# Kernel tuning notes

Hardware: AMD Instinct MI355X
Metric: run time of the kernel (lower is better)

Reference implementation:

```python
import jax, jax.numpy as jnp
import numpy as np

B, Q, MAXK, C, D, H, NL = 64, 16, 32, 64, 768, 512, 2
S = Q * (MAXK + 1) + 1  # max padded sequence length (529)


def lstm_layer(x, w_ih, w_hh, b_ih, b_hh):
    # x: [B, S, Din]; torch gate order i, f, g, o
    xg = jnp.einsum('bsd,gd->bsg', x, w_ih) + b_ih + b_hh  # [B,S,4H]
    h0 = jnp.zeros((x.shape[0], w_hh.shape[1]), x.dtype)

    def step(carry, xt):
        h, c = carry
        g = xt + h @ w_hh.T
        i, f, gg, o = jnp.split(g, 4, axis=-1)
        c = jax.nn.sigmoid(f) * c + jax.nn.sigmoid(i) * jnp.tanh(gg)
        h = jax.nn.sigmoid(o) * jnp.tanh(c)
        return (h, c), h

    _, hs = jax.lax.scan(step, (h0, h0), jnp.swapaxes(xg, 0, 1))
    return jnp.swapaxes(hs, 0, 1)  # [B,S,H]


def build_sequence(text_output, questions_outputs, code_embedding, num_snapshots, que_num):
    # Vectorized equivalent of the nested scatter loops.
    valid_q = jnp.arange(Q)[None, :] < que_num[:, None]          # [B,Q]
    qlen = jnp.where(valid_q, num_snapshots + 1, 0)              # per-question block length
    starts = jnp.cumsum(qlen, axis=1) - qlen                     # exclusive cumsum: block start
    L = jnp.sum(qlen, axis=1)                                    # text position; seq_len = L+1

    buf = jnp.zeros((B, S + 1, D), text_output.dtype)            # extra dump slot at index S
    b1 = jnp.arange(B)[:, None]

    # scatter question embeddings at block starts
    q_dest = jnp.where(valid_q, starts, S)
    buf = buf.at[b1, q_dest].set(questions_outputs)

    # scatter code snapshots: dest = start+1+k, src = code_embedding[b, i+k] (as in source)
    k = jnp.arange(MAXK)
    ns = jnp.where(valid_q, num_snapshots, 0)
    valid_s = k[None, None, :] < ns[:, :, None]                  # [B,Q,K]
    dest = jnp.where(valid_s, starts[:, :, None] + 1 + k[None, None, :], S)
    src = jnp.clip(jnp.arange(Q)[:, None] + k[None, :], 0, C - 1)  # [Q,K]
    code_vals = code_embedding[:, src]                           # [B,Q,K,D]
    buf = buf.at[jnp.arange(B)[:, None, None], dest].set(code_vals)

    # current-question text embedding at end of sequence
    buf = buf.at[jnp.arange(B), L].set(text_output)
    return buf[:, :S], L


def setup_inputs() -> dict:
    key = jax.random.key(0)
    ks = jax.random.split(key, 16)
    inp = {
        'text_output': jax.random.normal(ks[0], (B, D), jnp.float32),
        'questions_outputs': jax.random.normal(ks[1], (B, Q, D), jnp.float32),
        'code_embedding': jax.random.normal(ks[2], (B, C, D), jnp.float32),
        'num_snapshots': jax.random.randint(ks[3], (B, Q), 1, MAXK + 1, jnp.int32),
        'que_num': jax.random.randint(ks[4], (B,), 1, Q + 1, jnp.int32),
    }
    s = 0.02
    inp['w_ih_l0'] = jax.random.normal(ks[5], (4 * H, D), jnp.float32) * s
    inp['w_hh_l0'] = jax.random.normal(ks[6], (4 * H, H), jnp.float32) * s
    inp['b_ih_l0'] = jnp.zeros((4 * H,), jnp.float32)
    inp['b_hh_l0'] = jnp.zeros((4 * H,), jnp.float32)
    inp['w_ih_l1'] = jax.random.normal(ks[7], (4 * H, H), jnp.float32) * s
    inp['w_hh_l1'] = jax.random.normal(ks[8], (4 * H, H), jnp.float32) * s
    inp['b_ih_l1'] = jnp.zeros((4 * H,), jnp.float32)
    inp['b_hh_l1'] = jnp.zeros((4 * H,), jnp.float32)
    inp['fc_w'] = jax.random.normal(ks[9], (1, H), jnp.float32) * s
    inp['fc_b'] = jnp.zeros((1,), jnp.float32)
    return inp


def reference(text_output, questions_outputs, code_embedding, num_snapshots, que_num,
              w_ih_l0, w_hh_l0, b_ih_l0, b_hh_l0,
              w_ih_l1, w_hh_l1, b_ih_l1, b_hh_l1, fc_w, fc_b):
    x, L = build_sequence(text_output, questions_outputs, code_embedding, num_snapshots, que_num)
    h = lstm_layer(x, w_ih_l0, w_hh_l0, b_ih_l0, b_hh_l0)
    h = lstm_layer(h, w_ih_l1, w_hh_l1, b_ih_l1, b_hh_l1)
    last = h[jnp.arange(B), L]  # output at seq_len-1 (= text position)
    return last @ fc_w.T + fc_b  # [B, 1]
```

## Files before the change

kernel.cpp:

```cpp
#include <hip/hip_runtime.h>
#include <hip/hip_cooperative_groups.h>

namespace cg = cooperative_groups;

#define B_    64
#define Q_    16
#define MAXK_ 32
#define C_    64
#define D_    768
#define H_    512
#define G4_   2048
#define S_    529
#define NR_   81

typedef float f32x4_t __attribute__((ext_vector_type(4)));
typedef unsigned int u32x2_t __attribute__((ext_vector_type(2)));
typedef unsigned int u32x4_t __attribute__((ext_vector_type(4)));
typedef _Float16 f16x8_t __attribute__((ext_vector_type(8)));

static constexpr size_t OFF_L     = 0;
static constexpr size_t OFF_MAXL  = 256;
static constexpr size_t OFF_MAP   = 512;
static constexpr size_t OFF_BIAS0 = OFF_MAP   + 135424;
static constexpr size_t OFF_BIAS1 = OFF_BIAS0 + 8192;
static constexpr size_t OFF_C0    = OFF_BIAS1 + 8192;
static constexpr size_t OFF_C1    = OFF_C0    + 131072;
static constexpr size_t OFF_HLAST = OFF_C1    + 131072;
static constexpr size_t OFF_H0B   = OFF_HLAST + 131072;
static constexpr size_t OFF_H1B   = OFF_H0B   + 262144;
static constexpr size_t OFF_WTIH0 = OFF_H1B   + 262144;
static constexpr size_t OFF_XPROJ = OFF_WTIH0 + 6291456ULL;
static constexpr size_t OFF_BAR   = OFF_XPROJ + 42467328ULL;
static constexpr size_t OFF_ORD   = OFF_BAR   + 4096;
static constexpr size_t OFF_GMAX  = OFF_ORD   + 256;
static constexpr size_t WS_NEED   = OFF_GMAX  + 256;

__device__ __forceinline__ int group_base(int g) {
  return (g == 0) ? 0 : (g == 1) ? 16 : (g == 2) ? 48 : 32;
}

__device__ __forceinline__ void store_us_cc(ushort* p, unsigned int v) {
  asm volatile("global_store_short %0, %1, off sc0 sc1" :: "v"(p), "v"(v) : "memory");
}
__device__ __forceinline__ void store_f_cc(float* p, float v) {
  asm volatile("global_store_dword %0, %1, off sc0 sc1" :: "v"(p), "v"(v) : "memory");
}
__device__ __forceinline__ void load_a_cc(u32x4_t& v, const ushort* p) {
  asm volatile("global_load_dwordx4 %0, %1, off sc0 sc1" : "=v"(v) : "v"(p) : "memory");
}

__device__ __forceinline__ unsigned int pkrtz(float a, float b) {
  auto r = __builtin_amdgcn_cvt_pkrtz(a, b);
  unsigned int u;
  __builtin_memcpy(&u, &r, 4);
  return u;
}
__device__ __forceinline__ unsigned int f2h(float a) {
  return pkrtz(a, 0.f) & 0xffffu;
}
__device__ __forceinline__ f32x4_t mfma16(u32x4_t a, u32x4_t b, f32x4_t c) {
  f16x8_t av, bv;
  __builtin_memcpy(&av, &a, 16);
  __builtin_memcpy(&bv, &b, 16);
  return __builtin_amdgcn_mfma_f32_16x16x32_f16(av, bv, c, 0, 0, 0);
}

__device__ __forceinline__ float sigm(float x) { return 1.f/(1.f + __expf(-x)); }

__global__ __launch_bounds__(256) void k_prep(
    const int* __restrict__ ns, const int* __restrict__ que,
    const float* __restrict__ b_ih0, const float* __restrict__ b_hh0,
    const float* __restrict__ b_ih1, const float* __restrict__ b_hh1,
    int* __restrict__ Lp, int* __restrict__ maxLp, int* __restrict__ map,
    float* __restrict__ bias0, float* __restrict__ bias1,
    float* __restrict__ c0, float* __restrict__ c1, float* __restrict__ hlast,
    ushort* __restrict__ h0b, ushort* __restrict__ h1b, int* __restrict__ bar,
    int* __restrict__ ord, int* __restrict__ gmax)
{
  const int tid = threadIdx.x;
  for (int i = tid; i < B_*S_; i += 256) map[i] = -1;
  for (int i = tid; i < G4_; i += 256) {
    bias0[i] = b_ih0[i] + b_hh0[i];
    bias1[i] = b_ih1[i] + b_hh1[i];
  }
  int* h0i = (int*)h0b;
  int* h1i = (int*)h1b;
  for (int i = tid; i < B_*H_; i += 256) {
    c0[i]=0.f; c1[i]=0.f; hlast[i]=0.f;
    h0i[i]=0; h1i[i]=0;
  }
  for (int i = tid; i < 1024; i += 256) bar[i] = 0;
  if (tid == 0) *maxLp = 0;
  __syncthreads();
  if (tid < B_) {
    const int b = tid;
    const int qn = que[b];
    int pos = 0;
    int* m = map + b*S_;
    for (int q = 0; q < qn; ++q) {
      m[pos++] = q;
      const int n = ns[b*Q_ + q];
      for (int k = 0; k < n; ++k) {
        int j = q + k; if (j > C_-1) j = C_-1;
        m[pos++] = 16 + j;
      }
    }
    m[pos] = 80;
    Lp[b] = pos;
    atomicMax(maxLp, pos);
  }
  __syncthreads();
  if (tid < B_) {
    const int myL = Lp[tid];
    int rank = 0;
    for (int j = 0; j < B_; ++j) {
      const int lj = Lp[j];
      rank += (lj > myL) || (lj == myL && j < tid);
    }
    ord[rank] = tid;
  }
  __syncthreads();
  if (tid < 4) {
    const int gb = (tid == 0) ? 0 : (tid == 1) ? 16 : (tid == 2) ? 48 : 32;
    gmax[tid] = Lp[ord[gb]];
  }
}

__global__ __launch_bounds__(256) void k_transpose(
    const float* __restrict__ w, float* __restrict__ wT)
{
  __shared__ float tile[32][33];
  const int n0 = blockIdx.x * 32;
  const int k0 = blockIdx.y * 32;
  const int tx = threadIdx.x, ty = threadIdx.y;
  for (int i = ty; i < 32; i += 8)
    tile[i][tx] = w[(size_t)(n0+i)*D_ + k0 + tx];
  __syncthreads();
  for (int i = ty; i < 32; i += 8)
    wT[(size_t)(k0 + i)*G4_ + n0 + tx] = tile[tx][i];
}

__global__ __launch_bounds__(128, 2) void k_proj(
    const float* __restrict__ text, const float* __restrict__ ques,
    const float* __restrict__ code, const float* __restrict__ wT_ih0,
    const float* __restrict__ bias0, float* __restrict__ xproj)
{
  __shared__ float hsLds[32][64];
  const int mb = blockIdx.x, nb = blockIdx.y;
  const int n0 = nb * 128;
  const int tid = threadIdx.x;
  const int tb = tid >> 4, tn = tid & 15;
  const int b0 = tb * 8;
  const int bb = tid >> 1, hh = tid & 1;

  const int mrow = mb*64 + bb;
  const int sb = mrow / NR_, sr = mrow % NR_;
  const float* srcrow = (sr < 16) ? (ques + ((size_t)sb*Q_ + sr)*D_)
                      : (sr < 80) ? (code + ((size_t)sb*C_ + (sr-16))*D_)
                                  : (text + (size_t)sb*D_);

  float a[8][8];
  #pragma unroll
  for (int i=0;i<8;i++)
    #pragma unroll
    for (int j=0;j<8;j++) a[i][j]=0.f;

  for (int k0 = 0; k0 < D_; k0 += 32) {
    __syncthreads();
    {
      const float* p = srcrow + k0 + hh*16;
      float4 v0 = *(const float4*)(p+0);
      float4 v1 = *(const float4*)(p+4);
      float4 v2 = *(const float4*)(p+8);
      float4 v3 = *(const float4*)(p+12);
      const int kk = hh*16;
      hsLds[kk+ 0][bb]=v0.x; hsLds[kk+ 1][bb]=v0.y; hsLds[kk+ 2][bb]=v0.z; hsLds[kk+ 3][bb]=v0.w;
      hsLds[kk+ 4][bb]=v1.x; hsLds[kk+ 5][bb]=v1.y; hsLds[kk+ 6][bb]=v1.z; hsLds[kk+ 7][bb]=v1.w;
      hsLds[kk+ 8][bb]=v2.x; hsLds[kk+ 9][bb]=v2.y; hsLds[kk+10][bb]=v2.z; hsLds[kk+11][bb]=v2.w;
      hsLds[kk+12][bb]=v3.x; hsLds[kk+13][bb]=v3.y; hsLds[kk+14][bb]=v3.z; hsLds[kk+15][bb]=v3.w;
    }
    __syncthreads();
    const float* wb = wT_ih0 + (size_t)k0*G4_ + n0 + tn*8;
    #pragma unroll 4
    for (int k=0;k<32;k++){
      float4 w0 = *(const float4*)(wb + (size_t)k*G4_);
      float4 w1 = *(const float4*)(wb + (size_t)k*G4_ + 4);
      float4 hA = *(const float4*)(&hsLds[k][b0]);
      float4 hB = *(const float4*)(&hsLds[k][b0+4]);
      float hv[8]={hA.x,hA.y,hA.z,hA.w,hB.x,hB.y,hB.z,hB.w};
      float wv[8]={w0.x,w0.y,w0.z,w0.w,w1.x,w1.y,w1.z,w1.w};
      #pragma unroll
      for (int i=0;i<8;i++)
        #pragma unroll
        for (int j=0;j<8;j++)
          a[i][j] = fmaf(hv[i], wv[j], a[i][j]);
    }
  }
  float bz[8];
  #pragma unroll
  for (int j=0;j<8;j++) bz[j] = bias0[n0 + tn*8 + j];
  #pragma unroll
  for (int i=0;i<8;i++){
    const int m = mb*64 + b0 + i;
    float* pd = xproj + (size_t)m*G4_ + n0 + tn*8;
    *(float4*)(pd+0) = make_float4(a[i][0]+bz[0], a[i][1]+bz[1], a[i][2]+bz[2], a[i][3]+bz[3]);
    *(float4*)(pd+4) = make_float4(a[i][4]+bz[4], a[i][5]+bz[5], a[i][6]+bz[6], a[i][7]+bz[7]);
  }
}


__device__ __forceinline__ void load_wfrags(int tid, int us,
    const float* __restrict__ w_hh0, const float* __restrict__ w_ih1,
    const float* __restrict__ w_hh1, u32x4_t* wf0, u32x4_t* wf1)
{
  const int wv = tid >> 6, lane = tid & 63;
  const int nidx = lane & 15, kgrp = lane >> 4;
  const int ngl = (nidx >> 2)*H_ + us*4 + (nidx & 3);
  const float* r0 = w_hh0 + (size_t)ngl*H_ + wv*128 + kgrp*8;
  #pragma unroll
  for (int f = 0; f < 4; ++f) {
    float4 lo = *(const float4*)(r0 + f*32);
    float4 hi = *(const float4*)(r0 + f*32 + 4);
    wf0[f] = (u32x4_t){pkrtz(lo.x,lo.y), pkrtz(lo.z,lo.w), pkrtz(hi.x,hi.y), pkrtz(hi.z,hi.w)};
  }
  const float* w1 = (wv < 2) ? w_ih1 : w_hh1;
  const float* r1 = w1 + (size_t)ngl*H_ + (wv & 1)*256 + kgrp*8;
  #pragma unroll
  for (int f = 0; f < 8; ++f) {
    float4 lo = *(const float4*)(r1 + f*32);
    float4 hi = *(const float4*)(r1 + f*32 + 4);
    wf1[f] = (u32x4_t){pkrtz(lo.x,lo.y), pkrtz(lo.z,lo.w), pkrtz(hi.x,hi.y), pkrtz(hi.z,hi.w)};
  }
}

__device__ __forceinline__ void xg_prefetch(int t, int maxLg,
    const int* __restrict__ mrow, const float* __restrict__ xbase,
    float& xg0, float& xg1, float& xg2, float& xg3, int& rpre)
{
  rpre = (t <= maxLg) ? mrow[t] : -1;
  const float* xp = xbase + (size_t)(rpre < 0 ? 0 : rpre)*G4_;
  xg0 = xp[0]; xg1 = xp[512]; xg2 = xp[1024]; xg3 = xp[1536];
}

__device__ __forceinline__ void lstm_iter(int t, int maxLg, int gbase, int us,
    const u32x4_t* wf0, const u32x4_t* wf1, float* __restrict__ P,
    const ushort* __restrict__ h0c, ushort* __restrict__ h0n,
    const ushort* __restrict__ h1c, ushort* __restrict__ h1n,
    float* __restrict__ c0, float* __restrict__ c1, float* __restrict__ hlast,
    const int* __restrict__ mrow, const float* __restrict__ xbase,
    float& xg0, float& xg1, float& xg2, float& xg3, int& rpre0, int& rpre1,
    float b1v0, float b1v1, float b1v2, float b1v3, int Lrb, int rb)
{
  const int tid = threadIdx.x;
  const int wv = tid >> 6, lane = tid & 63;
  const int nidx = lane & 15, kgrp = lane >> 4;

  u32x4_t a0[4], a1[8];
  {
    const ushort* h0r = h0c + (size_t)(gbase + nidx)*H_ + wv*128 + kgrp*8;
    #pragma unroll
    for (int f = 0; f < 4; ++f) load_a_cc(a0[f], h0r + f*32);
    const ushort* hs1 = (wv < 2) ? h0c : h1c;
    const ushort* h1r = hs1 + (size_t)(gbase + nidx)*H_ + (wv & 1)*256 + kgrp*8;
    #pragma unroll
    for (int f = 0; f < 8; ++f) load_a_cc(a1[f], h1r + f*32);
  }
  asm volatile("s_waitcnt vmcnt(0)" ::: "memory");
  __builtin_amdgcn_sched_barrier(0);

  f32x4_t acc0 = {0.f,0.f,0.f,0.f};
  f32x4_t acc1 = {0.f,0.f,0.f,0.f};
  #pragma unroll
  for (int f = 0; f < 4; ++f) acc0 = mfma16(a0[f], wf0[f], acc0);
  #pragma unroll
  for (int f = 0; f < 8; ++f) acc1 = mfma16(a1[f], wf1[f], acc1);

  #pragma unroll
  for (int r = 0; r < 4; ++r) {
    P[((wv*2+0)*16 + kgrp*4 + r)*17 + nidx] = acc0[r];
    P[((wv*2+1)*16 + kgrp*4 + r)*17 + nidx] = acc1[r];
  }

  float nxg0=xg0, nxg1=xg1, nxg2=xg2, nxg3=xg3;
  int nr0 = -1, nr1 = -1;
  if (tid < 64) {
    xg_prefetch(t + 1, maxLg, mrow, xbase, nxg0, nxg1, nxg2, nxg3, nr0);
  } else if (tid < 128) {
    nr1 = (t <= maxLg) ? mrow[t] : -1;
  }
  __syncthreads();

  if (tid < 64) {
    if (rpre0 >= 0) {
      const int bl = tid & 15, ul = tid >> 4;
      const int pb = gbase + bl, u = us*4 + ul;
      const int idx = pb*H_ + u;
      float g0=xg0, g1=xg1, g2=xg2, g3=xg3;
      #pragma unroll
      for (int w = 0; w < 4; ++w) {
        const float* Pr = P + ((w*2+0)*16 + bl)*17 + ul;
        g0 += Pr[0]; g1 += Pr[4]; g2 += Pr[8]; g3 += Pr[12];
      }
      const float cc = sigm(g1)*c0[idx] + sigm(g0)*tanhf(g2);
      c0[idx] = cc;
      store_us_cc(h0n + idx, f2h(sigm(g3)*tanhf(cc)));
    }
  } else if (tid < 128) {
    if (rpre1 >= 0) {
      const int w2 = tid - 64;
      const int bl = w2 & 15, ul = w2 >> 4;
      const int pb = gbase + bl, u = us*4 + ul;
      const int idx = pb*H_ + u;
      float g0=b1v0, g1=b1v1, g2=b1v2, g3=b1v3;
      #pragma unroll
      for (int w = 0; w < 4; ++w) {
        const float* Pr = P + ((w*2+1)*16 + bl)*17 + ul;
        g0 += Pr[0]; g1 += Pr[4]; g2 += Pr[8]; g3 += Pr[12];
      }
      const float cc = sigm(g1)*c1[idx] + sigm(g0)*tanhf(g2);
      c1[idx] = cc;
      const float hn = sigm(g3)*tanhf(cc);
      store_us_cc(h1n + idx, f2h(hn));
      if (t - 1 == Lrb) store_f_cc(hlast + rb*H_ + u, hn);
    }
  }

  xg0 = nxg0; xg1 = nxg1; xg2 = nxg2; xg3 = nxg3;
  rpre0 = nr0; rpre1 = nr1;
}

__device__ __forceinline__ void grid_barrier_g(int* __restrict__ cnt, int gen)
{
  asm volatile("s_waitcnt vmcnt(0)" ::: "memory");
  __syncthreads();
  if (threadIdx.x == 0) {
    atomicAdd(cnt, 1);
    while (__hip_atomic_load(cnt, __ATOMIC_RELAXED, __HIP_MEMORY_SCOPE_AGENT) < gen*128)
      __builtin_amdgcn_s_sleep(1);
  }
  __syncthreads();
}

__global__ __launch_bounds__(256, 2) void k_lstm_coop(
    const float* __restrict__ w_hh0, const float* __restrict__ w_ih1,
    const float* __restrict__ w_hh1, const float* __restrict__ xproj,
    const float* __restrict__ bias1, const int* __restrict__ Lp,
    const int* __restrict__ gmax, const int* __restrict__ map,
    const int* __restrict__ ord,
    ushort* __restrict__ h0b, ushort* __restrict__ h1b,
    float* __restrict__ c0, float* __restrict__ c1, float* __restrict__ hlast,
    const float* __restrict__ fcw, const float* __restrict__ fcb,
    float* __restrict__ out, int* __restrict__ bar)
{
  __shared__ __align__(16) float P[8*16*17];
  const int blk = blockIdx.x;
  const int g = blk >> 7, us = blk & 127;
  const int gbase = group_base(g);
  const int tid = threadIdx.x;

  u32x4_t wf0[4], wf1[8];
  load_wfrags(tid, us, w_hh0, w_ih1, w_hh1, wf0, wf1);
  if (g < 2) __builtin_amdgcn_s_setprio(1);
  const int maxLg = gmax[g];
  int* cnt = bar + g*64;

  int rb = 0, Lrb = -2;
  const int* mrow = map;
  const float* xbase = xproj;
  float b1v0=0.f, b1v1=0.f, b1v2=0.f, b1v3=0.f;
  if (tid < 128) {
    rb = ord[gbase + (tid & 15)];
    mrow = map + rb*S_;
    if (tid < 64) {
      xbase = xproj + (size_t)rb*NR_*G4_ + (us*4 + (tid>>4));
    } else {
      const int u = us*4 + ((tid-64)>>4);
      b1v0=bias1[u]; b1v1=bias1[512+u]; b1v2=bias1[1024+u]; b1v3=bias1[1536+u];
      Lrb = Lp[rb];
    }
  }
  float xg0=0.f, xg1=0.f, xg2=0.f, xg3=0.f;
  int rpre0 = -1, rpre1 = -1;
  if (tid < 64) xg_prefetch(0, maxLg, mrow, xbase, xg0, xg1, xg2, xg3, rpre0);
  __syncthreads();

  for (int t = 0; t <= maxLg + 1; ++t) {
    const ushort* h0c = h0b + (size_t)(t & 1)*(B_*H_);
    ushort*       h0n = h0b + (size_t)((t+1) & 1)*(B_*H_);
    const ushort* h1c = h1b + (size_t)(t & 1)*(B_*H_);
    ushort*       h1n = h1b + (size_t)((t+1) & 1)*(B_*H_);
    lstm_iter(t, maxLg, gbase, us, wf0, wf1, P,
              h0c, h0n, h1c, h1n, c0, c1, hlast,
              mrow, xbase, xg0, xg1, xg2, xg3, rpre0, rpre1,
              b1v0, b1v1, b1v2, b1v3, Lrb, rb);
    grid_barrier_g(cnt, t + 1);
  }
  if (us == 0 && tid < 32) {
    const int pb = gbase + (tid >> 1), half = tid & 1;
    const int rbf = ord[pb];
    const float* hv = hlast + (size_t)rbf*H_ + half*256;
    const float* fw = fcw + half*256;
    float s = 0.f;
    #pragma unroll 8
    for (int u = 0; u < 256; ++u) s = fmaf(hv[u], fw[u], s);
    s += __shfl_xor(s, 1);
    if (half == 0) store_f_cc(out + rbf, s + fcb[0]);
  }
}

__global__ __launch_bounds__(256, 2) void k_step(int t,
    const float* __restrict__ w_hh0, const float* __restrict__ w_ih1,
    const float* __restrict__ w_hh1, const float* __restrict__ xproj,
    const float* __restrict__ bias1, const int* __restrict__ Lp,
    const int* __restrict__ gmax, const int* __restrict__ map,
    const int* __restrict__ ord,
    ushort* __restrict__ h0b, ushort* __restrict__ h1b,
    float* __restrict__ c0, float* __restrict__ c1, float* __restrict__ hlast)
{
  __shared__ __align__(16) float P[8*16*17];
  const int blk = blockIdx.x;
  const int g = blk >> 7, us = blk & 127;
  const int gbase = group_base(g);
  const int maxLg = gmax[g];
  if (t > maxLg + 1) return;
  const int tid = threadIdx.x;
  u32x4_t wf0[4], wf1[8];
  load_wfrags(tid, us, w_hh0, w_ih1, w_hh1, wf0, wf1);

  int rb = 0, Lrb = -2;
  const int* mrow = map;
  const float* xbase = xproj;
  float b1v0=0.f, b1v1=0.f, b1v2=0.f, b1v3=0.f;
  if (tid < 128) {
    rb = ord[gbase + (tid & 15)];
    mrow = map + rb*S_;
    if (tid < 64) {
      xbase = xproj + (size_t)rb*NR_*G4_ + (us*4 + (tid>>4));
    } else {
      const int u = us*4 + ((tid-64)>>4);
      b1v0=bias1[u]; b1v1=bias1[512+u]; b1v2=bias1[1024+u]; b1v3=bias1[1536+u];
      Lrb = Lp[rb];
    }
  }
  float xg0=0.f, xg1=0.f, xg2=0.f, xg3=0.f;
  int rpre0 = -1, rpre1 = -1;
  if (tid < 64) xg_prefetch(t, maxLg, mrow, xbase, xg0, xg1, xg2, xg3, rpre0);
  else if (tid < 128) rpre1 = (t-1 >= 0 && t-1 <= maxLg) ? mrow[t-1] : -1;
  __syncthreads();

  const ushort* h0c = h0b + (size_t)(t & 1)*(B_*H_);
  ushort*       h0n = h0b + (size_t)((t+1) & 1)*(B_*H_);
  const ushort* h1c = h1b + (size_t)(t & 1)*(B_*H_);
  ushort*       h1n = h1b + (size_t)((t+1) & 1)*(B_*H_);
  lstm_iter(t, maxLg, gbase, us, wf0, wf1, P,
            h0c, h0n, h1c, h1n, c0, c1, hlast,
            mrow, xbase, xg0, xg1, xg2, xg3, rpre0, rpre1,
            b1v0, b1v1, b1v2, b1v3, Lrb, rb);
}

__global__ __launch_bounds__(128) void k_fc(
    const float* __restrict__ hlast, const float* __restrict__ fcw,
    const float* __restrict__ fcb, float* __restrict__ out)
{
  const int tid = threadIdx.x;
  if (tid < 128) {
    const int b = tid >> 1, half = tid & 1;
    const float* hv = hlast + (size_t)b*H_ + half*256;
    const float* fw = fcw + half*256;
    float s = 0.f;
    #pragma unroll 8
    for (int u = 0; u < 256; ++u) s = fmaf(hv[u], fw[u], s);
    s += __shfl_xor(s, 1);
    if (half == 0) out[b] = s + fcb[0];
  }
}

extern "C" void kernel_launch(void* const* d_in, const int* in_sizes, int n_in,
                              void* d_out, int out_size, void* d_ws, size_t ws_size,
                              hipStream_t stream)
{
  const float* text  = (const float*)d_in[0];
  const float* ques  = (const float*)d_in[1];
  const float* code  = (const float*)d_in[2];
  const int*   ns    = (const int*)  d_in[3];
  const int*   que   = (const int*)  d_in[4];
  const float* w_ih0 = (const float*)d_in[5];
  const float* w_hh0 = (const float*)d_in[6];
  const float* b_ih0 = (const float*)d_in[7];
  const float* b_hh0 = (const float*)d_in[8];
  const float* w_ih1 = (const float*)d_in[9];
  const float* w_hh1 = (const float*)d_in[10];
  const float* b_ih1 = (const float*)d_in[11];
  const float* b_hh1 = (const float*)d_in[12];
  const float* fcw   = (const float*)d_in[13];
  const float* fcb   = (const float*)d_in[14];
  float* out = (float*)d_out;

  char* ws = (char*)d_ws;
  int*    Lp     = (int*)   (ws + OFF_L);
  int*    maxLp  = (int*)   (ws + OFF_MAXL);
  int*    map    = (int*)   (ws + OFF_MAP);
  float*  bias0  = (float*) (ws + OFF_BIAS0);
  float*  bias1  = (float*) (ws + OFF_BIAS1);
  float*  c0     = (float*) (ws + OFF_C0);
  float*  c1     = (float*) (ws + OFF_C1);
  float*  hlast  = (float*) (ws + OFF_HLAST);
  ushort* h0b    = (ushort*)(ws + OFF_H0B);
  ushort* h1b    = (ushort*)(ws + OFF_H1B);
  float*  wT_ih0 = (float*) (ws + OFF_WTIH0);
  float*  xproj  = (float*) (ws + OFF_XPROJ);
  int*    bar    = (int*)   (ws + OFF_BAR);
  int*    ord    = (int*)   (ws + OFF_ORD);
  int*    gmax   = (int*)   (ws + OFF_GMAX);
  (void)in_sizes; (void)n_in; (void)out_size; (void)ws_size; (void)WS_NEED;

  hipLaunchKernelGGL(k_prep, dim3(1), dim3(256), 0, stream,
                     ns, que, b_ih0, b_hh0, b_ih1, b_hh1,
                     Lp, maxLp, map, bias0, bias1, c0, c1, hlast, h0b, h1b, bar,
                     ord, gmax);

  hipLaunchKernelGGL(k_transpose, dim3(64, 24), dim3(32, 8), 0, stream,
                     w_ih0, wT_ih0);

  hipLaunchKernelGGL(k_proj, dim3(81, 16), dim3(128), 0, stream,
                     text, ques, code, wT_ih0, bias0, xproj);

  const float* a_whh0 = w_hh0; const float* a_wih1 = w_ih1; const float* a_whh1 = w_hh1;
  const float* a_xp = xproj;   const float* a_b1 = bias1;
  const int* a_Lp = Lp; const int* a_gmax = gmax; const int* a_map = map;
  const int* a_ord = ord;
  ushort* a_h0b = h0b; ushort* a_h1b = h1b; float* a_c0 = c0; float* a_c1 = c1;
  float* a_hl = hlast; const float* a_fcw = fcw; const float* a_fcb = fcb;
  float* a_out = out; int* a_bar = bar;
  void* args[] = { &a_whh0, &a_wih1, &a_whh1, &a_xp, &a_b1, &a_Lp, &a_gmax, &a_map,
                   &a_ord, &a_h0b, &a_h1b, &a_c0, &a_c1, &a_hl, &a_fcw, &a_fcb,
                   &a_out, &a_bar };

  hipError_t err = hipLaunchCooperativeKernel((const void*)k_lstm_coop,
                                              dim3(512), dim3(256), args, 0, stream);
  if (err != hipSuccess) {
    (void)hipGetLastError();
    for (int t = 0; t < S_ + 1; ++t) {
      hipLaunchKernelGGL(k_step, dim3(512), dim3(256), 0, stream, t,
                         w_hh0, w_ih1, w_hh1, xproj, bias1, Lp, gmax, map, ord,
                         h0b, h1b, c0, c1, hlast);
    }
    hipLaunchKernelGGL(k_fc, dim3(1), dim3(128), 0, stream, hlast, fcw, fcb, out);
  }
}
```

Measured before the change: 2.744 ms.

## Give each LSTM block 16 hidden units and shrink cooperative grid to 128 blocks

Each block in the persistent LSTM kernel now owns 16 hidden units instead of 4, keeping four times as many fp16 weight fragments in registers and running four MFMA column tiles per step. The grid drops from 512 to 128 blocks, so the per-step grid barrier waits on 32 blocks per group instead of 128, and all 256 threads now do gate math rather than 128. The cost is much higher register pressure (48 weight fragments per thread, launch bounds lowered to one block per SIMD group), fewer CUs in use, and a larger shared-memory partial buffer. The priority boost for early groups is also removed.

Result: faster. 2.255 ms (-17.8%).

```diff
diff --git a/kernel.cpp b/kernel.cpp
--- a/kernel.cpp
+++ b/kernel.cpp
@@ -67,6 +67,9 @@
 
 __device__ __forceinline__ float sigm(float x) { return 1.f/(1.f + __expf(-x)); }
 
+#define PSEG 1280
+#define PCOL 20
+
 __global__ __launch_bounds__(256) void k_prep(
     const int* __restrict__ ns, const int* __restrict__ que,
     const float* __restrict__ b_ih0, const float* __restrict__ b_hh0,
@@ -215,21 +218,24 @@
 {
   const int wv = tid >> 6, lane = tid & 63;
   const int nidx = lane & 15, kgrp = lane >> 4;
-  const int ngl = (nidx >> 2)*H_ + us*4 + (nidx & 3);
-  const float* r0 = w_hh0 + (size_t)ngl*H_ + wv*128 + kgrp*8;
-  #pragma unroll
-  for (int f = 0; f < 4; ++f) {
-    float4 lo = *(const float4*)(r0 + f*32);
-    float4 hi = *(const float4*)(r0 + f*32 + 4);
-    wf0[f] = (u32x4_t){pkrtz(lo.x,lo.y), pkrtz(lo.z,lo.w), pkrtz(hi.x,hi.y), pkrtz(hi.z,hi.w)};
-  }
-  const float* w1 = (wv < 2) ? w_ih1 : w_hh1;
-  const float* r1 = w1 + (size_t)ngl*H_ + (wv & 1)*256 + kgrp*8;
-  #pragma unroll
-  for (int f = 0; f < 8; ++f) {
-    float4 lo = *(const float4*)(r1 + f*32);
-    float4 hi = *(const float4*)(r1 + f*32 + 4);
-    wf1[f] = (u32x4_t){pkrtz(lo.x,lo.y), pkrtz(lo.z,lo.w), pkrtz(hi.x,hi.y), pkrtz(hi.z,hi.w)};
+  #pragma unroll
+  for (int nt = 0; nt < 4; ++nt) {
+    const int ngl = (nidx >> 2)*H_ + us*16 + nt*4 + (nidx & 3);
+    const float* r0 = w_hh0 + (size_t)ngl*H_ + wv*128 + kgrp*8;
+    #pragma unroll
+    for (int f = 0; f < 4; ++f) {
+      float4 lo = *(const float4*)(r0 + f*32);
+      float4 hi = *(const float4*)(r0 + f*32 + 4);
+      wf0[nt*4+f] = (u32x4_t){pkrtz(lo.x,lo.y), pkrtz(lo.z,lo.w), pkrtz(hi.x,hi.y), pkrtz(hi.z,hi.w)};
+    }
+    const float* w1 = (wv < 2) ? w_ih1 : w_hh1;
+    const float* r1 = w1 + (size_t)ngl*H_ + (wv & 1)*256 + kgrp*8;
+    #pragma unroll
+    for (int f = 0; f < 8; ++f) {
+      float4 lo = *(const float4*)(r1 + f*32);
+      float4 hi = *(const float4*)(r1 + f*32 + 4);
+      wf1[nt*8+f] = (u32x4_t){pkrtz(lo.x,lo.y), pkrtz(lo.z,lo.w), pkrtz(hi.x,hi.y), pkrtz(hi.z,hi.w)};
+    }
   }
 }
 
@@ -268,61 +274,60 @@
   asm volatile("s_waitcnt vmcnt(0)" ::: "memory");
   __builtin_amdgcn_sched_barrier(0);
 
-  f32x4_t acc0 = {0.f,0.f,0.f,0.f};
-  f32x4_t acc1 = {0.f,0.f,0.f,0.f};
-  #pragma unroll
-  for (int f = 0; f < 4; ++f) acc0 = mfma16(a0[f], wf0[f], acc0);
-  #pragma unroll
-  for (int f = 0; f < 8; ++f) acc1 = mfma16(a1[f], wf1[f], acc1);
-
-  #pragma unroll
-  for (int r = 0; r < 4; ++r) {
-    P[((wv*2+0)*16 + kgrp*4 + r)*17 + nidx] = acc0[r];
-    P[((wv*2+1)*16 + kgrp*4 + r)*17 + nidx] = acc1[r];
+  f32x4_t acc0[4], acc1[4];
+  #pragma unroll
+  for (int nt = 0; nt < 4; ++nt) { acc0[nt] = (f32x4_t){0.f,0.f,0.f,0.f}; acc1[nt] = (f32x4_t){0.f,0.f,0.f,0.f}; }
+  #pragma unroll
+  for (int nt = 0; nt < 4; ++nt)
+    #pragma unroll
+    for (int f = 0; f < 4; ++f) acc0[nt] = mfma16(a0[f], wf0[nt*4+f], acc0[nt]);
+  #pragma unroll
+  for (int nt = 0; nt < 4; ++nt)
+    #pragma unroll
+    for (int f = 0; f < 8; ++f) acc1[nt] = mfma16(a1[f], wf1[nt*8+f], acc1[nt]);
+
+  #pragma unroll
+  for (int nt = 0; nt < 4; ++nt) {
+    *(f32x4_t*)(P + (wv*2+0)*PSEG + (nt*16 + nidx)*PCOL + kgrp*4) = acc0[nt];
+    *(f32x4_t*)(P + (wv*2+1)*PSEG + (nt*16 + nidx)*PCOL + kgrp*4) = acc1[nt];
   }
 
   float nxg0=xg0, nxg1=xg1, nxg2=xg2, nxg3=xg3;
-  int nr0 = -1, nr1 = -1;
-  if (tid < 64) {
-    xg_prefetch(t + 1, maxLg, mrow, xbase, nxg0, nxg1, nxg2, nxg3, nr0);
-  } else if (tid < 128) {
-    nr1 = (t <= maxLg) ? mrow[t] : -1;
-  }
-  __syncthreads();
-
-  if (tid < 64) {
-    if (rpre0 >= 0) {
-      const int bl = tid & 15, ul = tid >> 4;
-      const int pb = gbase + bl, u = us*4 + ul;
-      const int idx = pb*H_ + u;
-      float g0=xg0, g1=xg1, g2=xg2, g3=xg3;
-      #pragma unroll
-      for (int w = 0; w < 4; ++w) {
-        const float* Pr = P + ((w*2+0)*16 + bl)*17 + ul;
-        g0 += Pr[0]; g1 += Pr[4]; g2 += Pr[8]; g3 += Pr[12];
-      }
-      const float cc = sigm(g1)*c0[idx] + sigm(g0)*tanhf(g2);
-      c0[idx] = cc;
-      store_us_cc(h0n + idx, f2h(sigm(g3)*tanhf(cc)));
-    }
-  } else if (tid < 128) {
-    if (rpre1 >= 0) {
-      const int w2 = tid - 64;
-      const int bl = w2 & 15, ul = w2 >> 4;
-      const int pb = gbase + bl, u = us*4 + ul;
-      const int idx = pb*H_ + u;
-      float g0=b1v0, g1=b1v1, g2=b1v2, g3=b1v3;
-      #pragma unroll
-      for (int w = 0; w < 4; ++w) {
-        const float* Pr = P + ((w*2+1)*16 + bl)*17 + ul;
-        g0 += Pr[0]; g1 += Pr[4]; g2 += Pr[8]; g3 += Pr[12];
-      }
-      const float cc = sigm(g1)*c1[idx] + sigm(g0)*tanhf(g2);
-      c1[idx] = cc;
-      const float hn = sigm(g3)*tanhf(cc);
-      store_us_cc(h1n + idx, f2h(hn));
-      if (t - 1 == Lrb) store_f_cc(hlast + rb*H_ + u, hn);
-    }
+  int nr0 = -1;
+  const int nr1 = rpre0;
+  xg_prefetch(t + 1, maxLg, mrow, xbase, nxg0, nxg1, nxg2, nxg3, nr0);
+  __syncthreads();
+
+  const int bl = tid & 15, ul = tid >> 4;
+  const int pb = gbase + bl;
+  const int u = us*16 + ul;
+  const int idx = pb*H_ + u;
+  const int clb = (ul >> 2)*16 + (ul & 3);
+  if (rpre0 >= 0) {
+    float g0=xg0, g1=xg1, g2=xg2, g3=xg3;
+    #pragma unroll
+    for (int w = 0; w < 4; ++w) {
+      const float* Pr = P + (w*2+0)*PSEG + bl;
+      g0 += Pr[(clb+ 0)*PCOL]; g1 += Pr[(clb+ 4)*PCOL];
+      g2 += Pr[(clb+ 8)*PCOL]; g3 += Pr[(clb+12)*PCOL];
+    }
+    const float cc = sigm(g1)*c0[idx] + sigm(g0)*tanhf(g2);
+    c0[idx] = cc;
+    store_us_cc(h0n + idx, f2h(sigm(g3)*tanhf(cc)));
+  }
+  if (rpre1 >= 0) {
+    float g0=b1v0, g1=b1v1, g2=b1v2, g3=b1v3;
+    #pragma unroll
+    for (int w = 0; w < 4; ++w) {
+      const float* Pr = P + (w*2+1)*PSEG + bl;
+      g0 += Pr[(clb+ 0)*PCOL]; g1 += Pr[(clb+ 4)*PCOL];
+      g2 += Pr[(clb+ 8)*PCOL]; g3 += Pr[(clb+12)*PCOL];
+    }
+    const float cc = sigm(g1)*c1[idx] + sigm(g0)*tanhf(g2);
+    c1[idx] = cc;
+    const float hn = sigm(g3)*tanhf(cc);
+    store_us_cc(h1n + idx, f2h(hn));
+    if (t - 1 == Lrb) store_f_cc(hlast + rb*H_ + u, hn);
   }
 
   xg0 = nxg0; xg1 = nxg1; xg2 = nxg2; xg3 = nxg3;
@@ -335,13 +340,13 @@
   __syncthreads();
   if (threadIdx.x == 0) {
     atomicAdd(cnt, 1);
-    while (__hip_atomic_load(cnt, __ATOMIC_RELAXED, __HIP_MEMORY_SCOPE_AGENT) < gen*128)
+    while (__hip_atomic_load(cnt, __ATOMIC_RELAXED, __HIP_MEMORY_SCOPE_AGENT) < gen*32)
       __builtin_amdgcn_s_sleep(1);
   }
   __syncthreads();
 }
 
-__global__ __launch_bounds__(256, 2) void k_lstm_coop(
+__global__ __launch_bounds__(256, 1) void k_lstm_coop(
     const float* __restrict__ w_hh0, const float* __restrict__ w_ih1,
     const float* __restrict__ w_hh1, const float* __restrict__ xproj,
     const float* __restrict__ bias1, const int* __restrict__ Lp,
@@ -352,36 +357,27 @@
     const float* __restrict__ fcw, const float* __restrict__ fcb,
     float* __restrict__ out, int* __restrict__ bar)
 {
-  __shared__ __align__(16) float P[8*16*17];
+  __shared__ __align__(16) float P[8*PSEG];
   const int blk = blockIdx.x;
-  const int g = blk >> 7, us = blk & 127;
+  const int g = blk >> 5, us = blk & 31;
   const int gbase = group_base(g);
   const int tid = threadIdx.x;
 
-  u32x4_t wf0[4], wf1[8];
+  u32x4_t wf0[16], wf1[32];
   load_wfrags(tid, us, w_hh0, w_ih1, w_hh1, wf0, wf1);
-  if (g < 2) __builtin_amdgcn_s_setprio(1);
   const int maxLg = gmax[g];
   int* cnt = bar + g*64;
 
-  int rb = 0, Lrb = -2;
-  const int* mrow = map;
-  const float* xbase = xproj;
-  float b1v0=0.f, b1v1=0.f, b1v2=0.f, b1v3=0.f;
-  if (tid < 128) {
-    rb = ord[gbase + (tid & 15)];
-    mrow = map + rb*S_;
-    if (tid < 64) {
-      xbase = xproj + (size_t)rb*NR_*G4_ + (us*4 + (tid>>4));
-    } else {
-      const int u = us*4 + ((tid-64)>>4);
-      b1v0=bias1[u]; b1v1=bias1[512+u]; b1v2=bias1[1024+u]; b1v3=bias1[1536+u];
-      Lrb = Lp[rb];
-    }
-  }
+  const int rb = ord[gbase + (tid & 15)];
+  const int* mrow = map + rb*S_;
+  const int u = us*16 + (tid >> 4);
+  const float* xbase = xproj + (size_t)rb*NR_*G4_ + u;
+  const float b1v0 = bias1[u], b1v1 = bias1[512+u], b1v2 = bias1[1024+u], b1v3 = bias1[1536+u];
+  const int Lrb = Lp[rb];
+
   float xg0=0.f, xg1=0.f, xg2=0.f, xg3=0.f;
   int rpre0 = -1, rpre1 = -1;
-  if (tid < 64) xg_prefetch(0, maxLg, mrow, xbase, xg0, xg1, xg2, xg3, rpre0);
+  xg_prefetch(0, maxLg, mrow, xbase, xg0, xg1, xg2, xg3, rpre0);
   __syncthreads();
 
   for (int t = 0; t <= maxLg + 1; ++t) {
@@ -402,13 +398,13 @@
     const float* fw = fcw + half*256;
     float s = 0.f;
     #pragma unroll 8
-    for (int u = 0; u < 256; ++u) s = fmaf(hv[u], fw[u], s);
+    for (int uu = 0; uu < 256; ++uu) s = fmaf(hv[uu], fw[uu], s);
     s += __shfl_xor(s, 1);
     if (half == 0) store_f_cc(out + rbf, s + fcb[0]);
   }
 }
 
-__global__ __launch_bounds__(256, 2) void k_step(int t,
+__global__ __launch_bounds__(256, 1) void k_step(int t,
     const float* __restrict__ w_hh0, const float* __restrict__ w_ih1,
     const float* __restrict__ w_hh1, const float* __restrict__ xproj,
     const float* __restrict__ bias1, const int* __restrict__ Lp,
@@ -417,35 +413,27 @@
     ushort* __restrict__ h0b, ushort* __restrict__ h1b,
     float* __restrict__ c0, float* __restrict__ c1, float* __restrict__ hlast)
 {
-  __shared__ __align__(16) float P[8*16*17];
+  __shared__ __align__(16) float P[8*PSEG];
   const int blk = blockIdx.x;
-  const int g = blk >> 7, us = blk & 127;
+  const int g = blk >> 5, us = blk & 31;
   const int gbase = group_base(g);
   const int maxLg = gmax[g];
   if (t > maxLg + 1) return;
   const int tid = threadIdx.x;
-  u32x4_t wf0[4], wf1[8];
+  u32x4_t wf0[16], wf1[32];
   load_wfrags(tid, us, w_hh0, w_ih1, w_hh1, wf0, wf1);
 
-  int rb = 0, Lrb = -2;
-  const int* mrow = map;
-  const float* xbase = xproj;
-  float b1v0=0.f, b1v1=0.f, b1v2=0.f, b1v3=0.f;
-  if (tid < 128) {
-    rb = ord[gbase + (tid & 15)];
-    mrow = map + rb*S_;
-    if (tid < 64) {
-      xbase = xproj + (size_t)rb*NR_*G4_ + (us*4 + (tid>>4));
-    } else {
-      const int u = us*4 + ((tid-64)>>4);
-      b1v0=bias1[u]; b1v1=bias1[512+u]; b1v2=bias1[1024+u]; b1v3=bias1[1536+u];
-      Lrb = Lp[rb];
-    }
-  }
+  const int rb = ord[gbase + (tid & 15)];
+  const int* mrow = map + rb*S_;
+  const int u = us*16 + (tid >> 4);
+  const float* xbase = xproj + (size_t)rb*NR_*G4_ + u;
+  const float b1v0 = bias1[u], b1v1 = bias1[512+u], b1v2 = bias1[1024+u], b1v3 = bias1[1536+u];
+  const int Lrb = Lp[rb];
+
   float xg0=0.f, xg1=0.f, xg2=0.f, xg3=0.f;
   int rpre0 = -1, rpre1 = -1;
-  if (tid < 64) xg_prefetch(t, maxLg, mrow, xbase, xg0, xg1, xg2, xg3, rpre0);
-  else if (tid < 128) rpre1 = (t-1 >= 0 && t-1 <= maxLg) ? mrow[t-1] : -1;
+  xg_prefetch(t, maxLg, mrow, xbase, xg0, xg1, xg2, xg3, rpre0);
+  rpre1 = (t-1 >= 0 && t-1 <= maxLg) ? mrow[t-1] : -1;
   __syncthreads();
 
   const ushort* h0c = h0b + (size_t)(t & 1)*(B_*H_);
@@ -537,11 +525,11 @@
                    &a_out, &a_bar };
 
   hipError_t err = hipLaunchCooperativeKernel((const void*)k_lstm_coop,
-                                              dim3(512), dim3(256), args, 0, stream);
+                                              dim3(128), dim3(256), args, 0, stream);
   if (err != hipSuccess) {
     (void)hipGetLastError();
     for (int t = 0; t < S_ + 1; ++t) {
-      hipLaunchKernelGGL(k_step, dim3(512), dim3(256), 0, stream, t,
+      hipLaunchKernelGGL(k_step, dim3(128), dim3(256), 0, stream, t,
                          w_hh0, w_ih1, w_hh1, xproj, bias1, Lp, gmax, map, ord,
                          h0b, h1b, c0, c1, hlast);
     }
```
